# Optimization experiments

Measured on AMD Instinct MI355X. Metric: run time of the kernel, lower is better.

Reference implementation:

```python
import jax, jax.numpy as jnp
import numpy as np

CODEBOOK_SIZE = 1024
COMMITMENT_COST = 0.25
ENTROPY_RATIO = 0.1
ENTROPY_TEMP = 0.01


def squared_euclidean_distance(a, b):
    # a: [N, D], b: [K, D] -> [N, K]
    a2 = jnp.sum(a * a, axis=1, keepdims=True)            # [N, 1]
    b2 = jnp.sum(b * b, axis=1)[None, :]                  # [1, K]
    return a2 + b2 - 2.0 * (a @ b.T)


def entropy_loss(affinity, temperature):
    # MaskGIT-style 'softmax' entropy loss
    flat = affinity.reshape(-1, affinity.shape[-1]) / temperature
    probs = jax.nn.softmax(flat, axis=-1)
    log_probs = jax.nn.log_softmax(flat + 1e-5, axis=-1)
    target_probs = probs
    avg_probs = jnp.mean(target_probs, axis=0)
    avg_entropy = -jnp.sum(avg_probs * jnp.log(avg_probs + 1e-5))
    sample_entropy = -jnp.mean(jnp.sum(target_probs * log_probs, axis=-1))
    return sample_entropy - avg_entropy


def setup_inputs() -> dict:
    key = jax.random.key(0)
    kx, kc = jax.random.split(key)
    d = 256
    x = jax.random.normal(kx, (32, 32, 32, 256), dtype=jnp.float32)
    # variance_scaling(scale=1.0, mode='fan_in', distribution='uniform') for
    # shape (K, D): fan_in = D, limit = sqrt(3 * scale / fan_in)
    lim = float(np.sqrt(3.0 / d))
    codebook = jax.random.uniform(kc, (CODEBOOK_SIZE, d), jnp.float32, -lim, lim)
    return {"x": x, "codebook": codebook}


def reference(x, codebook):
    flat = x.reshape(-1, x.shape[-1])                      # [N, D]
    dist = squared_euclidean_distance(flat, codebook)      # [N, K]
    encoding_indices = jnp.argmin(dist, axis=-1)           # [N]
    # one_hot @ codebook == gather of codebook rows (same math, no one-hot)
    quantized = jnp.take(codebook, encoding_indices, axis=0).reshape(x.shape)

    e_latent_loss = jnp.mean((jax.lax.stop_gradient(quantized) - x) ** 2) * COMMITMENT_COST
    q_latent_loss = jnp.mean((quantized - jax.lax.stop_gradient(x)) ** 2)
    ent_loss = entropy_loss(-dist, ENTROPY_TEMP) * ENTROPY_RATIO
    loss = (e_latent_loss + q_latent_loss + ent_loss).astype(jnp.float32)

    # straight-through estimator
    quantized_st = x + jax.lax.stop_gradient(quantized - x)
    return quantized_st, loss, encoding_indices.reshape(x.shape[:-1])
```

## Files before the change

kernel.cpp:

```cpp
#include <hip/hip_runtime.h>
#include <math.h>
#include <float.h>

#define D 256
#define K 1024
#define NROWS 32768
#define MARGIN 1.0f
#define MAXCAND 12

#define LOSS_OFF 8388608
#define IDX_OFF  8388609

typedef _Float16 h8 __attribute__((ext_vector_type(8)));
typedef float    v4f __attribute__((ext_vector_type(4)));
typedef const __attribute__((address_space(1))) unsigned int* gas_u32p;
typedef __attribute__((address_space(3))) unsigned int* las_u32p;

__device__ __forceinline__ float np_sq_block128(const float* a) {
    float r0 = __fmul_rn(a[0], a[0]);
    float r1 = __fmul_rn(a[1], a[1]);
    float r2 = __fmul_rn(a[2], a[2]);
    float r3 = __fmul_rn(a[3], a[3]);
    float r4 = __fmul_rn(a[4], a[4]);
    float r5 = __fmul_rn(a[5], a[5]);
    float r6 = __fmul_rn(a[6], a[6]);
    float r7 = __fmul_rn(a[7], a[7]);
    for (int i = 8; i < 128; i += 8) {
        r0 = __fadd_rn(r0, __fmul_rn(a[i + 0], a[i + 0]));
        r1 = __fadd_rn(r1, __fmul_rn(a[i + 1], a[i + 1]));
        r2 = __fadd_rn(r2, __fmul_rn(a[i + 2], a[i + 2]));
        r3 = __fadd_rn(r3, __fmul_rn(a[i + 3], a[i + 3]));
        r4 = __fadd_rn(r4, __fmul_rn(a[i + 4], a[i + 4]));
        r5 = __fadd_rn(r5, __fmul_rn(a[i + 5], a[i + 5]));
        r6 = __fadd_rn(r6, __fmul_rn(a[i + 6], a[i + 6]));
        r7 = __fadd_rn(r7, __fmul_rn(a[i + 7], a[i + 7]));
    }
    float tA = __fadd_rn(__fadd_rn(r0, r1), __fadd_rn(r2, r3));
    float tB = __fadd_rn(__fadd_rn(r4, r5), __fadd_rn(r6, r7));
    return __fadd_rn(tA, tB);
}

__global__ void vq_prep(const float* __restrict__ cb, float* __restrict__ b2,
                        h8* __restrict__ cfrag, float* __restrict__ avg_acc,
                        float* __restrict__ scal) {
    int tid = blockIdx.x * 256 + threadIdx.x;
    {
        int ln = tid & 15;
        int qd = (tid >> 4) & 3;
        int T  = (tid >> 6) & 63;
        int s  = tid >> 12;
        int k  = T * 16 + ln;
        const float* c = cb + (size_t)k * D + s * 32 + qd * 8;
        float4 v0 = *(const float4*)c;
        float4 v1 = *(const float4*)(c + 4);
        h8 f;
        f[0] = (_Float16)v0.x; f[1] = (_Float16)v0.y;
        f[2] = (_Float16)v0.z; f[3] = (_Float16)v0.w;
        f[4] = (_Float16)v1.x; f[5] = (_Float16)v1.y;
        f[6] = (_Float16)v1.z; f[7] = (_Float16)v1.w;
        cfrag[tid] = f;
    }
    if (tid < K) {
        const float* c = cb + (size_t)tid * D;
        b2[tid] = __fadd_rn(np_sq_block128(c), np_sq_block128(c + 128));
    }
    if (tid >= 1024 && tid < 2048) avg_acc[tid - 1024] = 0.f;
    if (tid >= 2048 && tid < 2050) scal[tid - 2048] = 0.f;
}

__global__ __launch_bounds__(256, 2)
void vq_mfma(const float* __restrict__ x, const float* __restrict__ cb,
             const h8* __restrict__ cfrag, const float* __restrict__ b2,
             float* __restrict__ avg_acc, float* __restrict__ scal,
             float* __restrict__ out)
{
    __shared__ __align__(16) h8 bbuf[4096];
    __shared__ float mred[4][32];
    __shared__ int   kred[4][32];
    __shared__ float sred[4][32];
    __shared__ float tred[4][32];
    __shared__ int   bkl[32];
    __shared__ int   candn[32];
    __shared__ int   candk[32][MAXCAND];
    __shared__ __align__(16) float xbuf[256];

    const int t   = threadIdx.x;
    const int w   = t >> 6;
    const int q   = w;
    const int l64 = t & 63;
    const int qd  = l64 >> 4;
    const int ln  = l64 & 15;
    const int r0  = blockIdx.x * 32;

    if (t < 32) candn[t] = 0;

    v4f acc[2][16];
    #pragma unroll
    for (int rt = 0; rt < 2; ++rt)
        #pragma unroll
        for (int tt = 0; tt < 16; ++tt) acc[rt][tt] = (v4f)0.f;

    const float* ab[2] = { x + (size_t)(r0 + ln) * D,
                           x + (size_t)(r0 + 16 + ln) * D };

    float4 pa[4];
    #pragma unroll
    for (int rt = 0; rt < 2; ++rt) {
        pa[2 * rt]     = *(const float4*)(ab[rt] + qd * 8);
        pa[2 * rt + 1] = *(const float4*)(ab[rt] + qd * 8 + 4);
    }

    for (int s = 0; s < 8; ++s) {
        #pragma unroll
        for (int kk = 0; kk < 16; ++kk) {
            int T = w * 16 + kk;
            const h8* gsrc = cfrag + ((size_t)(s * 64 + T)) * 64 + l64;
            __builtin_amdgcn_global_load_lds(
                (gas_u32p)(const void*)gsrc,
                (las_u32p)(void*)(bbuf + T * 64),
                16, 0, 0);
        }
        asm volatile("s_waitcnt vmcnt(0)" ::: "memory");

        h8 af[2];
        #pragma unroll
        for (int rt = 0; rt < 2; ++rt) {
            float4 a0 = pa[2 * rt], a1 = pa[2 * rt + 1];
            af[rt][0] = (_Float16)a0.x; af[rt][1] = (_Float16)a0.y;
            af[rt][2] = (_Float16)a0.z; af[rt][3] = (_Float16)a0.w;
            af[rt][4] = (_Float16)a1.x; af[rt][5] = (_Float16)a1.y;
            af[rt][6] = (_Float16)a1.z; af[rt][7] = (_Float16)a1.w;
        }
        if (s < 7) {
            #pragma unroll
            for (int rt = 0; rt < 2; ++rt) {
                pa[2 * rt]     = *(const float4*)(ab[rt] + (s + 1) * 32 + qd * 8);
                pa[2 * rt + 1] = *(const float4*)(ab[rt] + (s + 1) * 32 + qd * 8 + 4);
            }
        }
        #pragma unroll
        for (int tt = 0; tt < 16; ++tt) {
            h8 bf = bbuf[(16 * q + tt) * 64 + l64];
            acc[0][tt] = __builtin_amdgcn_mfma_f32_16x16x32_f16(af[0], bf, acc[0][tt], 0, 0, 0);
            acc[1][tt] = __builtin_amdgcn_mfma_f32_16x16x32_f16(af[1], bf, acc[1][tt], 0, 0, 0);
        }
    }

    float b2c[16];
    #pragma unroll
    for (int tt = 0; tt < 16; ++tt) b2c[tt] = b2[256 * q + 16 * tt + ln];
    #pragma unroll
    for (int rt = 0; rt < 2; ++rt)
        #pragma unroll
        for (int tt = 0; tt < 16; ++tt)
            #pragma unroll
            for (int r = 0; r < 4; ++r)
                acc[rt][tt][r] = 200.f * acc[rt][tt][r] - 100.f * b2c[tt];

    float m[2][4]; int bk[2][4];
    #pragma unroll
    for (int rt = 0; rt < 2; ++rt)
        #pragma unroll
        for (int r = 0; r < 4; ++r) { m[rt][r] = -INFINITY; bk[rt][r] = K; }
    #pragma unroll
    for (int tt = 0; tt < 16; ++tt)
        #pragma unroll
        for (int rt = 0; rt < 2; ++rt)
            #pragma unroll
            for (int r = 0; r < 4; ++r) {
                float z = acc[rt][tt][r];
                int code = 256 * q + 16 * tt + ln;
                if (z > m[rt][r]) { m[rt][r] = z; bk[rt][r] = code; }
            }
    #pragma unroll
    for (int off = 1; off < 16; off <<= 1)
        #pragma unroll
        for (int rt = 0; rt < 2; ++rt)
            #pragma unroll
            for (int r = 0; r < 4; ++r) {
                float om = __shfl_xor(m[rt][r], off);
                int   ok = __shfl_xor(bk[rt][r], off);
                if (om > m[rt][r] || (om == m[rt][r] && ok < bk[rt][r])) {
                    m[rt][r] = om; bk[rt][r] = ok;
                }
            }
    if (ln == 0)
        #pragma unroll
        for (int rt = 0; rt < 2; ++rt)
            #pragma unroll
            for (int r = 0; r < 4; ++r) {
                int rl = 16 * rt + 4 * qd + r;
                mred[q][rl] = m[rt][r]; kred[q][rl] = bk[rt][r];
            }
    __syncthreads();

    float mf[2][4]; int kf[2][4];
    #pragma unroll
    for (int rt = 0; rt < 2; ++rt)
        #pragma unroll
        for (int r = 0; r < 4; ++r) {
            int rl = 16 * rt + 4 * qd + r;
            mf[rt][r] = mred[0][rl]; kf[rt][r] = kred[0][rl];
            #pragma unroll
            for (int qq = 1; qq < 4; ++qq) {
                float mm = mred[qq][rl];
                if (mm > mf[rt][r]) { mf[rt][r] = mm; kf[rt][r] = kred[qq][rl]; }
            }
        }

    float S[2][4] = {{0,0,0,0},{0,0,0,0}}, T[2][4] = {{0,0,0,0},{0,0,0,0}};
    #pragma unroll
    for (int tt = 0; tt < 16; ++tt)
        #pragma unroll
        for (int rt = 0; rt < 2; ++rt)
            #pragma unroll
            for (int r = 0; r < 4; ++r) {
                float z  = acc[rt][tt][r];
                float zz = z - mf[rt][r];
                float e  = __expf(zz);
                if (z > mf[rt][r] - MARGIN) {
                    int rl = 16 * rt + 4 * qd + r;
                    int slot = atomicAdd(&candn[rl], 1);
                    if (slot < MAXCAND) candk[rl][slot] = 256 * q + 16 * tt + ln;
                }
                S[rt][r] += e; T[rt][r] += zz * e;
                acc[rt][tt][r] = e;
            }
    #pragma unroll
    for (int off = 1; off < 16; off <<= 1)
        #pragma unroll
        for (int rt = 0; rt < 2; ++rt)
            #pragma unroll
            for (int r = 0; r < 4; ++r) {
                S[rt][r] += __shfl_xor(S[rt][r], off);
                T[rt][r] += __shfl_xor(T[rt][r], off);
            }
    if (ln == 0)
        #pragma unroll
        for (int rt = 0; rt < 2; ++rt)
            #pragma unroll
            for (int r = 0; r < 4; ++r) {
                int rl = 16 * rt + 4 * qd + r;
                sred[q][rl] = S[rt][r]; tred[q][rl] = T[rt][r];
            }
    __syncthreads();

    float iS[2][4];
    float hsum = 0.f;
    #pragma unroll
    for (int rt = 0; rt < 2; ++rt)
        #pragma unroll
        for (int r = 0; r < 4; ++r) {
            int rl = 16 * rt + 4 * qd + r;
            float Sf = sred[0][rl] + sred[1][rl] + sred[2][rl] + sred[3][rl];
            float Tf = tred[0][rl] + tred[1][rl] + tred[2][rl] + tred[3][rl];
            iS[rt][r] = 1.f / Sf;
            if (q == 0 && ln == 0) {
                bkl[rl] = kf[rt][r];
                hsum += Tf * iS[rt][r] - __logf(Sf);
            }
        }
    if (q == 0 && ln == 0) atomicAdd(&scal[1], hsum);

    #pragma unroll
    for (int tt = 0; tt < 16; ++tt)
        #pragma unroll
        for (int rt = 0; rt < 2; ++rt)
            #pragma unroll
            for (int r = 0; r < 4; ++r) {
                float p = acc[rt][tt][r] * iS[rt][r];
                if (p > 1e-12f)
                    atomicAdd(&avg_acc[256 * q + 16 * tt + ln], p);
            }
    __syncthreads();

    if (w == 0) {
        for (int row = 0; row < 32; ++row) {
            int tc = candn[row];
            if (tc < 2) continue;
            if (tc > MAXCAND) tc = MAXCAND;
            const float* xr = x + (size_t)(r0 + row) * D;
            *(float4*)&xbuf[l64 * 4] = *(const float4*)(xr + l64 * 4);
            float a2f = __fadd_rn(np_sq_block128(xbuf), np_sq_block128(xbuf + 128));
            float bestd = FLT_MAX; int bestk = K;
            for (int c = 0; c < tc; ++c) {
                int k = candk[row][c];
                double sdot = 0.0;
                #pragma unroll
                for (int dd = 0; dd < 4; ++dd)
                    sdot += (double)cb[(size_t)k * D + l64 * 4 + dd] *
                            (double)xbuf[l64 * 4 + dd];
                #pragma unroll
                for (int off = 32; off > 0; off >>= 1)
                    sdot += __shfl_xor(sdot, off);
                float abf = (float)sdot;
                float dnp = __fsub_rn(__fadd_rn(a2f, b2[k]), __fmul_rn(2.0f, abf));
                if (dnp < bestd || (dnp == bestd && k < bestk)) {
                    bestd = dnp; bestk = k;
                }
            }
            if (l64 == 0) bkl[row] = bestk;
        }
    }
    __syncthreads();

    float wmse = 0.f;
    #pragma unroll
    for (int rr = 0; rr < 8; ++rr) {
        int rl  = 8 * w + rr;
        int row = r0 + rl;
        int bk2 = bkl[rl];
        float4 xv = *(const float4*)(x  + (size_t)row * D + l64 * 4);
        float4 qv = *(const float4*)(cb + (size_t)bk2 * D + l64 * 4);
        float dx = qv.x - xv.x, dy = qv.y - xv.y, dz = qv.z - xv.z, dw = qv.w - xv.w;
        float4 st;
        st.x = xv.x + dx; st.y = xv.y + dy; st.z = xv.z + dz; st.w = xv.w + dw;
        *(float4*)(out + (size_t)row * D + l64 * 4) = st;
        if (l64 == 0) out[IDX_OFF + row] = (float)bk2;
        wmse += dx * dx + dy * dy + dz * dz + dw * dw;
    }
    #pragma unroll
    for (int off = 32; off > 0; off >>= 1)
        wmse += __shfl_xor(wmse, off);
    if (l64 == 0) atomicAdd(&scal[0], wmse);
}

__global__ __launch_bounds__(1024)
void vq_fin(const float* __restrict__ avg_acc, const float* __restrict__ scal,
            float* __restrict__ out)
{
    __shared__ float sred[16];
    int t = threadIdx.x;
    float ap = avg_acc[t] * (1.f / 32768.f);
    float v = ap * logf(ap + 1e-5f);
    #pragma unroll
    for (int off = 32; off > 0; off >>= 1) v += __shfl_xor(v, off);
    if ((t & 63) == 0) sred[t >> 6] = v;
    __syncthreads();
    if (t == 0) {
        float s = 0.f;
        for (int w = 0; w < 16; ++w) s += sred[w];
        float avg_entropy = -s;
        float sampleH = -scal[1] * (1.f / 32768.f);
        float mse = scal[0] * (1.f / 8388608.f);
        float loss = 1.25f * mse + 0.1f * (sampleH - avg_entropy);
        out[LOSS_OFF] = loss;
    }
}

extern "C" void kernel_launch(void* const* d_in, const int* in_sizes, int n_in,
                              void* d_out, int out_size, void* d_ws, size_t ws_size,
                              hipStream_t stream)
{
    const float* x  = (const float*)d_in[0];
    const float* cb = (const float*)d_in[1];
    float* out = (float*)d_out;
    float* ws  = (float*)d_ws;
    float* b2      = ws;
    float* avg_acc = ws + K;
    float* scal    = ws + 2 * K;
    h8*    cfrag   = (h8*)((char*)d_ws + 16384);

    vq_prep<<<128, 256, 0, stream>>>(cb, b2, cfrag, avg_acc, scal);
    vq_mfma<<<NROWS / 32, 256, 0, stream>>>(x, cb, cfrag, b2, avg_acc, scal, out);
    vq_fin<<<1, 1024, 0, stream>>>(avg_acc, scal, out);
}
```

Measured before the change: 202.7 us.

## Halve rows per block, read codebook fragments directly, parallelize rescoring across waves

```diff
diff --git a/kernel.cpp b/kernel.cpp
--- a/kernel.cpp
+++ b/kernel.cpp
@@ -5,6 +5,7 @@
 #define D 256
 #define K 1024
 #define NROWS 32768
+#define ROWS 16
 #define MARGIN 1.0f
 #define MAXCAND 12
 
@@ -13,8 +14,6 @@
 
 typedef _Float16 h8 __attribute__((ext_vector_type(8)));
 typedef float    v4f __attribute__((ext_vector_type(4)));
-typedef const __attribute__((address_space(1))) unsigned int* gas_u32p;
-typedef __attribute__((address_space(3))) unsigned int* las_u32p;
 
 __device__ __forceinline__ float np_sq_block128(const float* a) {
     float r0 = __fmul_rn(a[0], a[0]);
@@ -68,21 +67,20 @@
     if (tid >= 2048 && tid < 2050) scal[tid - 2048] = 0.f;
 }
 
-__global__ __launch_bounds__(256, 2)
+__global__ __launch_bounds__(256, 4)
 void vq_mfma(const float* __restrict__ x, const float* __restrict__ cb,
              const h8* __restrict__ cfrag, const float* __restrict__ b2,
              float* __restrict__ avg_acc, float* __restrict__ scal,
              float* __restrict__ out)
 {
-    __shared__ __align__(16) h8 bbuf[4096];
-    __shared__ float mred[4][32];
-    __shared__ int   kred[4][32];
-    __shared__ float sred[4][32];
-    __shared__ float tred[4][32];
-    __shared__ int   bkl[32];
-    __shared__ int   candn[32];
-    __shared__ int   candk[32][MAXCAND];
-    __shared__ __align__(16) float xbuf[256];
+    __shared__ float mred[4][ROWS];
+    __shared__ int   kred[4][ROWS];
+    __shared__ float sred[4][ROWS];
+    __shared__ float tred[4][ROWS];
+    __shared__ int   bkl[ROWS];
+    __shared__ int   candn[ROWS];
+    __shared__ int   candk[ROWS][MAXCAND];
+    __shared__ __align__(16) float xbw[4][256];
 
     const int t   = threadIdx.x;
     const int w   = t >> 6;
@@ -90,224 +88,175 @@
     const int l64 = t & 63;
     const int qd  = l64 >> 4;
     const int ln  = l64 & 15;
-    const int r0  = blockIdx.x * 32;
-
-    if (t < 32) candn[t] = 0;
-
-    v4f acc[2][16];
-    #pragma unroll
-    for (int rt = 0; rt < 2; ++rt)
-        #pragma unroll
-        for (int tt = 0; tt < 16; ++tt) acc[rt][tt] = (v4f)0.f;
-
-    const float* ab[2] = { x + (size_t)(r0 + ln) * D,
-                           x + (size_t)(r0 + 16 + ln) * D };
-
-    float4 pa[4];
-    #pragma unroll
-    for (int rt = 0; rt < 2; ++rt) {
-        pa[2 * rt]     = *(const float4*)(ab[rt] + qd * 8);
-        pa[2 * rt + 1] = *(const float4*)(ab[rt] + qd * 8 + 4);
-    }
+    const int r0  = blockIdx.x * ROWS;
+
+    if (t < ROWS) candn[t] = 0;
+
+    v4f acc[16];
+    #pragma unroll
+    for (int tt = 0; tt < 16; ++tt) acc[tt] = (v4f)0.f;
+
+    const float* ab = x + (size_t)(r0 + ln) * D + qd * 8;
+
+    float4 pa0 = *(const float4*)(ab);
+    float4 pa1 = *(const float4*)(ab + 4);
 
     for (int s = 0; s < 8; ++s) {
-        #pragma unroll
-        for (int kk = 0; kk < 16; ++kk) {
-            int T = w * 16 + kk;
-            const h8* gsrc = cfrag + ((size_t)(s * 64 + T)) * 64 + l64;
-            __builtin_amdgcn_global_load_lds(
-                (gas_u32p)(const void*)gsrc,
-                (las_u32p)(void*)(bbuf + T * 64),
-                16, 0, 0);
-        }
-        asm volatile("s_waitcnt vmcnt(0)" ::: "memory");
-
-        h8 af[2];
-        #pragma unroll
-        for (int rt = 0; rt < 2; ++rt) {
-            float4 a0 = pa[2 * rt], a1 = pa[2 * rt + 1];
-            af[rt][0] = (_Float16)a0.x; af[rt][1] = (_Float16)a0.y;
-            af[rt][2] = (_Float16)a0.z; af[rt][3] = (_Float16)a0.w;
-            af[rt][4] = (_Float16)a1.x; af[rt][5] = (_Float16)a1.y;
-            af[rt][6] = (_Float16)a1.z; af[rt][7] = (_Float16)a1.w;
-        }
+        h8 af;
+        af[0] = (_Float16)pa0.x; af[1] = (_Float16)pa0.y;
+        af[2] = (_Float16)pa0.z; af[3] = (_Float16)pa0.w;
+        af[4] = (_Float16)pa1.x; af[5] = (_Float16)pa1.y;
+        af[6] = (_Float16)pa1.z; af[7] = (_Float16)pa1.w;
         if (s < 7) {
+            pa0 = *(const float4*)(ab + (s + 1) * 32);
+            pa1 = *(const float4*)(ab + (s + 1) * 32 + 4);
+        }
+        const h8* bq = cfrag + ((size_t)(s * 64 + 16 * q)) * 64 + l64;
+        #pragma unroll
+        for (int tt = 0; tt < 16; ++tt) {
+            h8 bf = bq[(size_t)tt * 64];
+            acc[tt] = __builtin_amdgcn_mfma_f32_16x16x32_f16(af, bf, acc[tt], 0, 0, 0);
+        }
+    }
+
+    float b2c[16];
+    #pragma unroll
+    for (int tt = 0; tt < 16; ++tt) b2c[tt] = b2[256 * q + 16 * tt + ln];
+    #pragma unroll
+    for (int tt = 0; tt < 16; ++tt)
+        #pragma unroll
+        for (int r = 0; r < 4; ++r)
+            acc[tt][r] = 200.f * acc[tt][r] - 100.f * b2c[tt];
+
+    float m[4]; int bk[4];
+    #pragma unroll
+    for (int r = 0; r < 4; ++r) { m[r] = -INFINITY; bk[r] = K; }
+    #pragma unroll
+    for (int tt = 0; tt < 16; ++tt)
+        #pragma unroll
+        for (int r = 0; r < 4; ++r) {
+            float z = acc[tt][r];
+            int code = 256 * q + 16 * tt + ln;
+            if (z > m[r]) { m[r] = z; bk[r] = code; }
+        }
+    #pragma unroll
+    for (int off = 1; off < 16; off <<= 1)
+        #pragma unroll
+        for (int r = 0; r < 4; ++r) {
+            float om = __shfl_xor(m[r], off);
+            int   ok = __shfl_xor(bk[r], off);
+            if (om > m[r] || (om == m[r] && ok < bk[r])) { m[r] = om; bk[r] = ok; }
+        }
+    if (ln == 0)
+        #pragma unroll
+        for (int r = 0; r < 4; ++r) {
+            int rl = 4 * qd + r;
+            mred[q][rl] = m[r]; kred[q][rl] = bk[r];
+        }
+    __syncthreads();
+
+    float mf[4]; int kf[4];
+    #pragma unroll
+    for (int r = 0; r < 4; ++r) {
+        int rl = 4 * qd + r;
+        mf[r] = mred[0][rl]; kf[r] = kred[0][rl];
+        #pragma unroll
+        for (int qq = 1; qq < 4; ++qq) {
+            float mm = mred[qq][rl];
+            if (mm > mf[r]) { mf[r] = mm; kf[r] = kred[qq][rl]; }
+        }
+    }
+
+    float S[4] = {0, 0, 0, 0}, T[4] = {0, 0, 0, 0};
+    #pragma unroll
+    for (int tt = 0; tt < 16; ++tt)
+        #pragma unroll
+        for (int r = 0; r < 4; ++r) {
+            float z  = acc[tt][r];
+            float zz = z - mf[r];
+            float e  = __expf(zz);
+            if (z > mf[r] - MARGIN) {
+                int rl = 4 * qd + r;
+                int slot = atomicAdd(&candn[rl], 1);
+                if (slot < MAXCAND) candk[rl][slot] = 256 * q + 16 * tt + ln;
+            }
+            S[r] += e; T[r] += zz * e;
+            acc[tt][r] = e;
+        }
+    #pragma unroll
+    for (int off = 1; off < 16; off <<= 1)
+        #pragma unroll
+        for (int r = 0; r < 4; ++r) {
+            S[r] += __shfl_xor(S[r], off);
+            T[r] += __shfl_xor(T[r], off);
+        }
+    if (ln == 0)
+        #pragma unroll
+        for (int r = 0; r < 4; ++r) {
+            int rl = 4 * qd + r;
+            sred[q][rl] = S[r]; tred[q][rl] = T[r];
+        }
+    __syncthreads();
+
+    float iS[4];
+    float hsum = 0.f;
+    #pragma unroll
+    for (int r = 0; r < 4; ++r) {
+        int rl = 4 * qd + r;
+        float Sf = sred[0][rl] + sred[1][rl] + sred[2][rl] + sred[3][rl];
+        float Tf = tred[0][rl] + tred[1][rl] + tred[2][rl] + tred[3][rl];
+        iS[r] = 1.f / Sf;
+        if (q == 0 && ln == 0) {
+            bkl[rl] = kf[r];
+            hsum += Tf * iS[r] - __logf(Sf);
+        }
+    }
+    if (q == 0 && ln == 0) atomicAdd(&scal[1], hsum);
+
+    #pragma unroll
+    for (int tt = 0; tt < 16; ++tt)
+        #pragma unroll
+        for (int r = 0; r < 4; ++r) {
+            float p = acc[tt][r] * iS[r];
+            if (p > 1e-12f)
+                atomicAdd(&avg_acc[256 * q + 16 * tt + ln], p);
+        }
+    __syncthreads();
+
+    for (int j = 0; j < 4; ++j) {
+        int rl = 4 * w + j;
+        int tc = candn[rl];
+        if (tc < 2) continue;
+        if (tc > MAXCAND) tc = MAXCAND;
+        const float* xr = x + (size_t)(r0 + rl) * D;
+        *(float4*)&xbw[w][l64 * 4] = *(const float4*)(xr + l64 * 4);
+        float a2f = __fadd_rn(np_sq_block128((const float*)xbw[w]),
+                              np_sq_block128((const float*)xbw[w] + 128));
+        float bestd = FLT_MAX; int bestk = K;
+        for (int c = 0; c < tc; ++c) {
+            int k = candk[rl][c];
+            double sdot = 0.0;
             #pragma unroll
-            for (int rt = 0; rt < 2; ++rt) {
-                pa[2 * rt]     = *(const float4*)(ab[rt] + (s + 1) * 32 + qd * 8);
-                pa[2 * rt + 1] = *(const float4*)(ab[rt] + (s + 1) * 32 + qd * 8 + 4);
+            for (int dd = 0; dd < 4; ++dd)
+                sdot += (double)cb[(size_t)k * D + l64 * 4 + dd] *
+                        (double)xbw[w][l64 * 4 + dd];
+            #pragma unroll
+            for (int off = 32; off > 0; off >>= 1)
+                sdot += __shfl_xor(sdot, off);
+            float abf = (float)sdot;
+            float dnp = __fsub_rn(__fadd_rn(a2f, b2[k]), __fmul_rn(2.0f, abf));
+            if (dnp < bestd || (dnp == bestd && k < bestk)) {
+                bestd = dnp; bestk = k;
             }
         }
-        #pragma unroll
-        for (int tt = 0; tt < 16; ++tt) {
-            h8 bf = bbuf[(16 * q + tt) * 64 + l64];
-            acc[0][tt] = __builtin_amdgcn_mfma_f32_16x16x32_f16(af[0], bf, acc[0][tt], 0, 0, 0);
-            acc[1][tt] = __builtin_amdgcn_mfma_f32_16x16x32_f16(af[1], bf, acc[1][tt], 0, 0, 0);
-        }
-    }
-
-    float b2c[16];
-    #pragma unroll
-    for (int tt = 0; tt < 16; ++tt) b2c[tt] = b2[256 * q + 16 * tt + ln];
-    #pragma unroll
-    for (int rt = 0; rt < 2; ++rt)
-        #pragma unroll
-        for (int tt = 0; tt < 16; ++tt)
-            #pragma unroll
-            for (int r = 0; r < 4; ++r)
-                acc[rt][tt][r] = 200.f * acc[rt][tt][r] - 100.f * b2c[tt];
-
-    float m[2][4]; int bk[2][4];
-    #pragma unroll
-    for (int rt = 0; rt < 2; ++rt)
-        #pragma unroll
-        for (int r = 0; r < 4; ++r) { m[rt][r] = -INFINITY; bk[rt][r] = K; }
-    #pragma unroll
-    for (int tt = 0; tt < 16; ++tt)
-        #pragma unroll
-        for (int rt = 0; rt < 2; ++rt)
-            #pragma unroll
-            for (int r = 0; r < 4; ++r) {
-                float z = acc[rt][tt][r];
-                int code = 256 * q + 16 * tt + ln;
-                if (z > m[rt][r]) { m[rt][r] = z; bk[rt][r] = code; }
-            }
-    #pragma unroll
-    for (int off = 1; off < 16; off <<= 1)
-        #pragma unroll
-        for (int rt = 0; rt < 2; ++rt)
-            #pragma unroll
-            for (int r = 0; r < 4; ++r) {
-                float om = __shfl_xor(m[rt][r], off);
-                int   ok = __shfl_xor(bk[rt][r], off);
-                if (om > m[rt][r] || (om == m[rt][r] && ok < bk[rt][r])) {
-                    m[rt][r] = om; bk[rt][r] = ok;
-                }
-            }
-    if (ln == 0)
-        #pragma unroll
-        for (int rt = 0; rt < 2; ++rt)
-            #pragma unroll
-            for (int r = 0; r < 4; ++r) {
-                int rl = 16 * rt + 4 * qd + r;
-                mred[q][rl] = m[rt][r]; kred[q][rl] = bk[rt][r];
-            }
-    __syncthreads();
-
-    float mf[2][4]; int kf[2][4];
-    #pragma unroll
-    for (int rt = 0; rt < 2; ++rt)
-        #pragma unroll
-        for (int r = 0; r < 4; ++r) {
-            int rl = 16 * rt + 4 * qd + r;
-            mf[rt][r] = mred[0][rl]; kf[rt][r] = kred[0][rl];
-            #pragma unroll
-            for (int qq = 1; qq < 4; ++qq) {
-                float mm = mred[qq][rl];
-                if (mm > mf[rt][r]) { mf[rt][r] = mm; kf[rt][r] = kred[qq][rl]; }
-            }
-        }
-
-    float S[2][4] = {{0,0,0,0},{0,0,0,0}}, T[2][4] = {{0,0,0,0},{0,0,0,0}};
-    #pragma unroll
-    for (int tt = 0; tt < 16; ++tt)
-        #pragma unroll
-        for (int rt = 0; rt < 2; ++rt)
-            #pragma unroll
-            for (int r = 0; r < 4; ++r) {
-                float z  = acc[rt][tt][r];
-                float zz = z - mf[rt][r];
-                float e  = __expf(zz);
-                if (z > mf[rt][r] - MARGIN) {
-                    int rl = 16 * rt + 4 * qd + r;
-                    int slot = atomicAdd(&candn[rl], 1);
-                    if (slot < MAXCAND) candk[rl][slot] = 256 * q + 16 * tt + ln;
-                }
-                S[rt][r] += e; T[rt][r] += zz * e;
-                acc[rt][tt][r] = e;
-            }
-    #pragma unroll
-    for (int off = 1; off < 16; off <<= 1)
-        #pragma unroll
-        for (int rt = 0; rt < 2; ++rt)
-            #pragma unroll
-            for (int r = 0; r < 4; ++r) {
-                S[rt][r] += __shfl_xor(S[rt][r], off);
-                T[rt][r] += __shfl_xor(T[rt][r], off);
-            }
-    if (ln == 0)
-        #pragma unroll
-        for (int rt = 0; rt < 2; ++rt)
-            #pragma unroll
-            for (int r = 0; r < 4; ++r) {
-                int rl = 16 * rt + 4 * qd + r;
-                sred[q][rl] = S[rt][r]; tred[q][rl] = T[rt][r];
-            }
-    __syncthreads();
-
-    float iS[2][4];
-    float hsum = 0.f;
-    #pragma unroll
-    for (int rt = 0; rt < 2; ++rt)
-        #pragma unroll
-        for (int r = 0; r < 4; ++r) {
-            int rl = 16 * rt + 4 * qd + r;
-            float Sf = sred[0][rl] + sred[1][rl] + sred[2][rl] + sred[3][rl];
-            float Tf = tred[0][rl] + tred[1][rl] + tred[2][rl] + tred[3][rl];
-            iS[rt][r] = 1.f / Sf;
-            if (q == 0 && ln == 0) {
-                bkl[rl] = kf[rt][r];
-                hsum += Tf * iS[rt][r] - __logf(Sf);
-            }
-        }
-    if (q == 0 && ln == 0) atomicAdd(&scal[1], hsum);
-
-    #pragma unroll
-    for (int tt = 0; tt < 16; ++tt)
-        #pragma unroll
-        for (int rt = 0; rt < 2; ++rt)
-            #pragma unroll
-            for (int r = 0; r < 4; ++r) {
-                float p = acc[rt][tt][r] * iS[rt][r];
-                if (p > 1e-12f)
-                    atomicAdd(&avg_acc[256 * q + 16 * tt + ln], p);
-            }
-    __syncthreads();
-
-    if (w == 0) {
-        for (int row = 0; row < 32; ++row) {
-            int tc = candn[row];
-            if (tc < 2) continue;
-            if (tc > MAXCAND) tc = MAXCAND;
-            const float* xr = x + (size_t)(r0 + row) * D;
-            *(float4*)&xbuf[l64 * 4] = *(const float4*)(xr + l64 * 4);
-            float a2f = __fadd_rn(np_sq_block128(xbuf), np_sq_block128(xbuf + 128));
-            float bestd = FLT_MAX; int bestk = K;
-            for (int c = 0; c < tc; ++c) {
-                int k = candk[row][c];
-                double sdot = 0.0;
-                #pragma unroll
-                for (int dd = 0; dd < 4; ++dd)
-                    sdot += (double)cb[(size_t)k * D + l64 * 4 + dd] *
-                            (double)xbuf[l64 * 4 + dd];
-                #pragma unroll
-                for (int off = 32; off > 0; off >>= 1)
-                    sdot += __shfl_xor(sdot, off);
-                float abf = (float)sdot;
-                float dnp = __fsub_rn(__fadd_rn(a2f, b2[k]), __fmul_rn(2.0f, abf));
-                if (dnp < bestd || (dnp == bestd && k < bestk)) {
-                    bestd = dnp; bestk = k;
-                }
-            }
-            if (l64 == 0) bkl[row] = bestk;
-        }
+        if (l64 == 0) bkl[rl] = bestk;
     }
     __syncthreads();
 
     float wmse = 0.f;
     #pragma unroll
-    for (int rr = 0; rr < 8; ++rr) {
-        int rl  = 8 * w + rr;
+    for (int rr = 0; rr < 4; ++rr) {
+        int rl  = 4 * w + rr;
         int row = r0 + rl;
         int bk2 = bkl[rl];
         float4 xv = *(const float4*)(x  + (size_t)row * D + l64 * 4);
@@ -362,6 +311,6 @@
     h8*    cfrag   = (h8*)((char*)d_ws + 16384);
 
     vq_prep<<<128, 256, 0, stream>>>(cb, b2, cfrag, avg_acc, scal);
-    vq_mfma<<<NROWS / 32, 256, 0, stream>>>(x, cb, cfrag, b2, avg_acc, scal, out);
+    vq_mfma<<<NROWS / ROWS, 256, 0, stream>>>(x, cb, cfrag, b2, avg_acc, scal, out);
     vq_fin<<<1, 1024, 0, stream>>>(avg_acc, scal, out);
 }
```

Result: slower. 254.5 us (+25.6%).

## Load codebook MFMA fragments directly from global memory instead of staging through LDS

Applied to the files above, without the earlier changes.

```diff
diff --git a/kernel.cpp b/kernel.cpp
--- a/kernel.cpp
+++ b/kernel.cpp
@@ -13,27 +13,29 @@
 
 typedef _Float16 h8 __attribute__((ext_vector_type(8)));
 typedef float    v4f __attribute__((ext_vector_type(4)));
-typedef const __attribute__((address_space(1))) unsigned int* gas_u32p;
-typedef __attribute__((address_space(3))) unsigned int* las_u32p;
 
 __device__ __forceinline__ float np_sq_block128(const float* a) {
-    float r0 = __fmul_rn(a[0], a[0]);
-    float r1 = __fmul_rn(a[1], a[1]);
-    float r2 = __fmul_rn(a[2], a[2]);
-    float r3 = __fmul_rn(a[3], a[3]);
-    float r4 = __fmul_rn(a[4], a[4]);
-    float r5 = __fmul_rn(a[5], a[5]);
-    float r6 = __fmul_rn(a[6], a[6]);
-    float r7 = __fmul_rn(a[7], a[7]);
+    float4 v0 = *(const float4*)a;
+    float4 v1 = *(const float4*)(a + 4);
+    float r0 = __fmul_rn(v0.x, v0.x);
+    float r1 = __fmul_rn(v0.y, v0.y);
+    float r2 = __fmul_rn(v0.z, v0.z);
+    float r3 = __fmul_rn(v0.w, v0.w);
+    float r4 = __fmul_rn(v1.x, v1.x);
+    float r5 = __fmul_rn(v1.y, v1.y);
+    float r6 = __fmul_rn(v1.z, v1.z);
+    float r7 = __fmul_rn(v1.w, v1.w);
     for (int i = 8; i < 128; i += 8) {
-        r0 = __fadd_rn(r0, __fmul_rn(a[i + 0], a[i + 0]));
-        r1 = __fadd_rn(r1, __fmul_rn(a[i + 1], a[i + 1]));
-        r2 = __fadd_rn(r2, __fmul_rn(a[i + 2], a[i + 2]));
-        r3 = __fadd_rn(r3, __fmul_rn(a[i + 3], a[i + 3]));
-        r4 = __fadd_rn(r4, __fmul_rn(a[i + 4], a[i + 4]));
-        r5 = __fadd_rn(r5, __fmul_rn(a[i + 5], a[i + 5]));
-        r6 = __fadd_rn(r6, __fmul_rn(a[i + 6], a[i + 6]));
-        r7 = __fadd_rn(r7, __fmul_rn(a[i + 7], a[i + 7]));
+        float4 u0 = *(const float4*)(a + i);
+        float4 u1 = *(const float4*)(a + i + 4);
+        r0 = __fadd_rn(r0, __fmul_rn(u0.x, u0.x));
+        r1 = __fadd_rn(r1, __fmul_rn(u0.y, u0.y));
+        r2 = __fadd_rn(r2, __fmul_rn(u0.z, u0.z));
+        r3 = __fadd_rn(r3, __fmul_rn(u0.w, u0.w));
+        r4 = __fadd_rn(r4, __fmul_rn(u1.x, u1.x));
+        r5 = __fadd_rn(r5, __fmul_rn(u1.y, u1.y));
+        r6 = __fadd_rn(r6, __fmul_rn(u1.z, u1.z));
+        r7 = __fadd_rn(r7, __fmul_rn(u1.w, u1.w));
     }
     float tA = __fadd_rn(__fadd_rn(r0, r1), __fadd_rn(r2, r3));
     float tB = __fadd_rn(__fadd_rn(r4, r5), __fadd_rn(r6, r7));
@@ -74,7 +76,6 @@
              float* __restrict__ avg_acc, float* __restrict__ scal,
              float* __restrict__ out)
 {
-    __shared__ __align__(16) h8 bbuf[4096];
     __shared__ float mred[4][32];
     __shared__ int   kred[4][32];
     __shared__ float sred[4][32];
@@ -111,17 +112,6 @@
     }
 
     for (int s = 0; s < 8; ++s) {
-        #pragma unroll
-        for (int kk = 0; kk < 16; ++kk) {
-            int T = w * 16 + kk;
-            const h8* gsrc = cfrag + ((size_t)(s * 64 + T)) * 64 + l64;
-            __builtin_amdgcn_global_load_lds(
-                (gas_u32p)(const void*)gsrc,
-                (las_u32p)(void*)(bbuf + T * 64),
-                16, 0, 0);
-        }
-        asm volatile("s_waitcnt vmcnt(0)" ::: "memory");
-
         h8 af[2];
         #pragma unroll
         for (int rt = 0; rt < 2; ++rt) {
@@ -138,40 +128,33 @@
                 pa[2 * rt + 1] = *(const float4*)(ab[rt] + (s + 1) * 32 + qd * 8 + 4);
             }
         }
+        const h8* bq = cfrag + ((size_t)(s * 64 + 16 * q)) * 64 + l64;
         #pragma unroll
         for (int tt = 0; tt < 16; ++tt) {
-            h8 bf = bbuf[(16 * q + tt) * 64 + l64];
+            h8 bf = bq[(size_t)tt * 64];
             acc[0][tt] = __builtin_amdgcn_mfma_f32_16x16x32_f16(af[0], bf, acc[0][tt], 0, 0, 0);
             acc[1][tt] = __builtin_amdgcn_mfma_f32_16x16x32_f16(af[1], bf, acc[1][tt], 0, 0, 0);
         }
     }
 
-    float b2c[16];
-    #pragma unroll
-    for (int tt = 0; tt < 16; ++tt) b2c[tt] = b2[256 * q + 16 * tt + ln];
+    float m[2][4]; int bk[2][4];
     #pragma unroll
     for (int rt = 0; rt < 2; ++rt)
         #pragma unroll
-        for (int tt = 0; tt < 16; ++tt)
-            #pragma unroll
-            for (int r = 0; r < 4; ++r)
-                acc[rt][tt][r] = 200.f * acc[rt][tt][r] - 100.f * b2c[tt];
-
-    float m[2][4]; int bk[2][4];
-    #pragma unroll
-    for (int rt = 0; rt < 2; ++rt)
-        #pragma unroll
         for (int r = 0; r < 4; ++r) { m[rt][r] = -INFINITY; bk[rt][r] = K; }
     #pragma unroll
-    for (int tt = 0; tt < 16; ++tt)
-        #pragma unroll
-        for (int rt = 0; rt < 2; ++rt)
-            #pragma unroll
-            for (int r = 0; r < 4; ++r) {
-                float z = acc[rt][tt][r];
-                int code = 256 * q + 16 * tt + ln;
+    for (int tt = 0; tt < 16; ++tt) {
+        float b2v = b2[256 * q + 16 * tt + ln];
+        int code = 256 * q + 16 * tt + ln;
+        #pragma unroll
+        for (int rt = 0; rt < 2; ++rt)
+            #pragma unroll
+            for (int r = 0; r < 4; ++r) {
+                float z = 200.f * acc[rt][tt][r] - 100.f * b2v;
+                acc[rt][tt][r] = z;
                 if (z > m[rt][r]) { m[rt][r] = z; bk[rt][r] = code; }
             }
+    }
     #pragma unroll
     for (int off = 1; off < 16; off <<= 1)
         #pragma unroll
```

Result: slower. 207.1 us (+2.1%).
